# Kernel tuning notes

Hardware: AMD Instinct MI355X
Metric: run time of the kernel (lower is better)

The kernel has to match this reference:

```python
import jax, jax.numpy as jnp
import numpy as np

B = 512      # batch
H = 64       # latent_dim == GRU hidden size
F = 32       # n_features
S = 2048     # seq_len
NEG_SLOPE = 0.01  # nn.LeakyReLU default


def setup_inputs() -> dict:
    key = jax.random.key(0)
    ks = jax.random.split(key, 14)

    def p(k, shape, scale=0.1):
        return jax.random.normal(k, shape, dtype=jnp.float32) * scale

    return {
        "noise": jax.random.normal(ks[0], (B, H), dtype=jnp.float32),
        # GRU forward direction (layer 0): weight_ih_l0, weight_hh_l0, biases
        "W_ih_f": p(ks[1], (3 * H, H)),
        "W_hh_f": p(ks[2], (3 * H, H)),
        "b_ih_f": p(ks[3], (3 * H,)),
        "b_hh_f": p(ks[4], (3 * H,)),
        # GRU backward direction (layer 0 reverse)
        "W_ih_b": p(ks[5], (3 * H, H)),
        "W_hh_b": p(ks[6], (3 * H, H)),
        "b_ih_b": p(ks[7], (3 * H,)),
        "b_hh_b": p(ks[8], (3 * H,)),
        # latent_linear: Linear(2H -> H)
        "W_lat": p(ks[9], (H, 2 * H)),
        "b_lat": p(ks[10], (H,)),
        # output_linear: Linear(H -> F)
        "W_out": p(ks[11], (F, H)),
        "b_out": p(ks[12], (F,)),
    }


def _leaky(x):
    return jnp.where(x >= 0, x, NEG_SLOPE * x)


def _gru_cell(x, h, W_ih, W_hh, b_ih, b_hh):
    # PyTorch GRU cell: gates ordered (r, z, n)
    gi = x @ W_ih.T + b_ih          # (B, 3H)
    gh = h @ W_hh.T + b_hh          # (B, 3H)
    i_r, i_z, i_n = jnp.split(gi, 3, axis=-1)
    h_r, h_z, h_n = jnp.split(gh, 3, axis=-1)
    r = jax.nn.sigmoid(i_r + h_r)
    z = jax.nn.sigmoid(i_z + h_z)
    n = jnp.tanh(i_n + r * h_n)
    return (1.0 - z) * n + z * h


def reference(noise, W_ih_f, W_hh_f, b_ih_f, b_hh_f,
              W_ih_b, W_hh_b, b_ih_b, b_hh_b,
              W_lat, b_lat, W_out, b_out):
    # hidden_state = noise.repeat((D*n_layers,1,1)) -> both directions start at noise
    batch = noise.shape[0]

    def step(carry, _):
        x, hf, hb = carry
        # GRU on a length-1 sequence: each direction does one cell update;
        # output timestep = concat(fwd_out, bwd_out)
        hf2 = _gru_cell(x, hf, W_ih_f, W_hh_f, b_ih_f, b_hh_f)
        hb2 = _gru_cell(x, hb, W_ih_b, W_hh_b, b_ih_b, b_hh_b)
        out = jnp.concatenate([hf2, hb2], axis=-1)        # (B, 2H)
        lat = _leaky(out @ W_lat.T + b_lat)               # (B, H)
        return (lat, hf2, hb2), lat

    x0 = jnp.zeros((batch, H), dtype=noise.dtype)
    _, ys = jax.lax.scan(step, (x0, noise, noise), None, length=S)
    seq = jnp.transpose(ys, (1, 0, 2))   # (B, S, H)
    seq = _leaky(seq)                    # second LeakyReLU as in the original
    out = jax.nn.sigmoid(seq @ W_out.T + b_out)  # (B, S, F)
    return out
```

## Files before the change

### kernel.cpp

```cpp
#include <hip/hip_runtime.h>
#include <hip/hip_bf16.h>


#define NBATCH 512
#define NH 64
#define NS 2048
#define NF 32
#define MROW 16
#define LDH 72

typedef short s16x8 __attribute__((ext_vector_type(8)));
typedef float f32x4 __attribute__((ext_vector_type(4)));

#define MFMA(a, b, c) __builtin_amdgcn_mfma_f32_16x16x32_bf16((a), (b), (c), 0, 0, 0)

#define NLOG2E  (-1.4426950408889634f)
#define N2LOG2E (-2.8853900817779268f)

__device__ __forceinline__ void bar_nodrain() {
    asm volatile("s_barrier" ::: "memory");
}

__device__ __forceinline__ void bar_lgkm() {
    asm volatile("s_waitcnt lgkmcnt(0)\n\ts_barrier" ::: "memory");
}

__device__ __forceinline__ short f2bf(float f) {
    return (short)((__float_as_uint(f) + 0x8000u) >> 16);
}

__device__ __forceinline__ f32x4 v_exp2(f32x4 a) {
    f32x4 r;
#pragma unroll
    for (int i = 0; i < 4; ++i) r[i] = __builtin_amdgcn_exp2f(a[i]);
    return r;
}

__device__ __forceinline__ f32x4 v_rcp(f32x4 a) {
    f32x4 r;
#pragma unroll
    for (int i = 0; i < 4; ++i) r[i] = __builtin_amdgcn_rcpf(a[i]);
    return r;
}

__device__ __forceinline__ f32x4 v_lk(f32x4 a) {
    f32x4 b = a * 0.01f;
    f32x4 r;
#pragma unroll
    for (int i = 0; i < 4; ++i) r[i] = fmaxf(a[i], b[i]);
    return r;
}

__device__ __forceinline__ f32x4 v_sigm(f32x4 a) {
    return v_rcp(v_exp2(a * NLOG2E) + 1.0f);
}

__device__ __forceinline__ int2 pk4bf(f32x4 v) {
    union { __hip_bfloat162 b; int i; } lo, hi;
    float2 a; a.x = v[0]; a.y = v[1];
    float2 b; b.x = v[2]; b.y = v[3];
    lo.b = __float22bfloat162_rn(a);
    hi.b = __float22bfloat162_rn(b);
    int2 r; r.x = lo.i; r.y = hi.i;
    return r;
}

__device__ __forceinline__ s16x8 bfragW(const float* __restrict__ W, int ldk,
                                        int row, int kf, int quad) {
    const float* p = W + (size_t)row * ldk + kf * 32 + quad * 8;
    s16x8 r;
#pragma unroll
    for (int i = 0; i < 8; ++i) r[i] = f2bf(p[i]);
    return r;
}

__device__ __forceinline__ f32x4 bias4(const float* __restrict__ p) {
    const float4 v = *(const float4*)p;
    f32x4 r = {v.x, v.y, v.z, v.w};
    return r;
}

__global__ __launch_bounds__(768)
void grugan_kernel(const float* __restrict__ noise,
                   const float* __restrict__ Wihf, const float* __restrict__ Whhf,
                   const float* __restrict__ bihf, const float* __restrict__ bhhf,
                   const float* __restrict__ Wihb, const float* __restrict__ Whhb,
                   const float* __restrict__ bihb, const float* __restrict__ bhhb,
                   const float* __restrict__ Wlat, const float* __restrict__ blat,
                   const float* __restrict__ Wout, const float* __restrict__ bout,
                   float* __restrict__ out)
{
    __shared__ __align__(16) short Xs[2][MROW][LDH];
    __shared__ __align__(16) short X2s[2][MROW][LDH];
    __shared__ __align__(16) short Hs[2][2][MROW][LDH];

    const int tid  = threadIdx.x;
    const int wave = tid >> 6;
    const int lane = tid & 63;
    const int n    = lane & 15;
    const int quad = lane >> 4;
    const int row0 = blockIdx.x * MROW;

    for (int idx = tid; idx < MROW * LDH; idx += 768) (&Xs[0][0][0])[idx] = 0;
    f32x4 hreg = {0.f, 0.f, 0.f, 0.f};
    const int gdir = wave >> 2;
    const int gjq  = (wave & 3) * 16 + quad * 4;
    if (wave < 8) {
        const float4 nz = *(const float4*)&noise[(size_t)(row0 + n) * NH + gjq];
        hreg[0] = nz.x; hreg[1] = nz.y; hreg[2] = nz.z; hreg[3] = nz.w;
        *(int2*)&Hs[0][gdir][n][gjq] = pk4bf(hreg);
    }
    __syncthreads();

    if (wave < 8) {
        const int dir  = gdir;
        const int cb   = wave & 3;
        const int jrow = cb * 16 + n;
        const int jq   = gjq;
        const float* Wih = dir ? Wihb : Wihf;
        const float* Whh = dir ? Whhb : Whhf;
        const float* bih = dir ? bihb : bihf;
        const float* bhh = dir ? bhhb : bhhf;

        s16x8 wir0 = bfragW(Wih, NH,   0 + jrow, 0, quad);
        s16x8 wir1 = bfragW(Wih, NH,   0 + jrow, 1, quad);
        s16x8 wiz0 = bfragW(Wih, NH,  64 + jrow, 0, quad);
        s16x8 wiz1 = bfragW(Wih, NH,  64 + jrow, 1, quad);
        s16x8 win0 = bfragW(Wih, NH, 128 + jrow, 0, quad);
        s16x8 win1 = bfragW(Wih, NH, 128 + jrow, 1, quad);
        s16x8 whr0 = bfragW(Whh, NH,   0 + jrow, 0, quad);
        s16x8 whr1 = bfragW(Whh, NH,   0 + jrow, 1, quad);
        s16x8 whz0 = bfragW(Whh, NH,  64 + jrow, 0, quad);
        s16x8 whz1 = bfragW(Whh, NH,  64 + jrow, 1, quad);
        s16x8 whn0 = bfragW(Whh, NH, 128 + jrow, 0, quad);
        s16x8 whn1 = bfragW(Whh, NH, 128 + jrow, 1, quad);
        f32x4 initR, initZ;
        {
            f32x4 a = bias4(&bih[jq]),      b = bias4(&bhh[jq]);
            initR = a + b;
            f32x4 c = bias4(&bih[64 + jq]), d = bias4(&bhh[64 + jq]);
            initZ = c + d;
        }
        const f32x4 initN1 = bias4(&bih[128 + jq]);
        const f32x4 initN2 = bias4(&bhh[128 + jq]);

        f32x4 accR, accZ, accN2;
        {
            s16x8 ha0 = *(const s16x8*)&Hs[0][dir][n][quad * 8];
            s16x8 ha1 = *(const s16x8*)&Hs[0][dir][n][32 + quad * 8];
            accR  = MFMA(whr0, ha0, initR);  accR  = MFMA(whr1, ha1, accR);
            accZ  = MFMA(whz0, ha0, initZ);  accZ  = MFMA(whz1, ha1, accZ);
            accN2 = MFMA(whn0, ha0, initN2); accN2 = MFMA(whn1, ha1, accN2);
        }

#define GSTEP(HB) do {                                                          \
        s16x8 xa0 = *(const s16x8*)&Xs[HB][n][quad * 8];                        \
        s16x8 xa1 = *(const s16x8*)&Xs[HB][n][32 + quad * 8];                   \
        accR = MFMA(wir0, xa0, accR);   accR = MFMA(wir1, xa1, accR);           \
        accZ = MFMA(wiz0, xa0, accZ);   accZ = MFMA(wiz1, xa1, accZ);           \
        f32x4 accN1 = MFMA(win0, xa0, initN1);                                  \
        accN1 = MFMA(win1, xa1, accN1);                                         \
        f32x4 eR = v_exp2(accR * NLOG2E);                                       \
        f32x4 rr = v_rcp(eR + 1.0f);                                            \
        f32x4 u  = accN1 + rr * accN2;                                          \
        f32x4 eU = v_exp2(u * N2LOG2E);                                         \
        f32x4 eZ = v_exp2(accZ * NLOG2E);                                       \
        f32x4 numer = (eZ + hreg) + eU * (hreg - eZ);                           \
        f32x4 denom = (eU + 1.0f) * (eZ + 1.0f);                                \
        hreg = numer * v_rcp(denom);                                            \
        *(int2*)&Hs[(HB) ^ 1][dir][n][jq] = pk4bf(hreg);                        \
        __syncthreads();                                \
        {                                                                       \
            s16x8 ha0 = *(const s16x8*)&Hs[(HB) ^ 1][dir][n][quad * 8];         \
            s16x8 ha1 = *(const s16x8*)&Hs[(HB) ^ 1][dir][n][32 + quad * 8];    \
            accR  = MFMA(whr0, ha0, initR);  accR  = MFMA(whr1, ha1, accR);     \
            accZ  = MFMA(whz0, ha0, initZ);  accZ  = MFMA(whz1, ha1, accZ);     \
            accN2 = MFMA(whn0, ha0, initN2); accN2 = MFMA(whn1, ha1, accN2);    \
        }                                                                       \
        __syncthreads();                                \
    } while (0)

        for (int t = 0; t < NS; t += 2) {
            GSTEP(0);
            GSTEP(1);
        }
#undef GSTEP
    } else {
        const int lt = wave & 3;
        const int nq = lt * 16 + quad * 4;
        s16x8 wl0 = bfragW(Wlat, 2 * NH, lt * 16 + n, 0, quad);
        s16x8 wl1 = bfragW(Wlat, 2 * NH, lt * 16 + n, 1, quad);
        s16x8 wl2 = bfragW(Wlat, 2 * NH, lt * 16 + n, 2, quad);
        s16x8 wl3 = bfragW(Wlat, 2 * NH, lt * 16 + n, 3, quad);
        const f32x4 initL = bias4(&blat[lt * 16 + quad * 4]);

        s16x8 wo0 = {};
        s16x8 wo1 = {};
        f32x4 initO = {0.f, 0.f, 0.f, 0.f};
        float* orow = nullptr;
        if (lt < 2) {
            const int f0 = lt * 16;
            wo0   = bfragW(Wout, NH, f0 + n, 0, quad);
            wo1   = bfragW(Wout, NH, f0 + n, 1, quad);
            initO = bias4(&bout[f0 + quad * 4]);
            orow  = out + (size_t)(row0 + n) * (NS * NF) + f0 + quad * 4;
        }
        const f32x4 zero4 = {0.f, 0.f, 0.f, 0.f};

#define LOSTEP(HB, T) do {                                                      \
        if (lt < 2 && (T) > 0) {                                                \
                \
                 \
            s16x8 p0 = *(const s16x8*)&X2s[HB][n][quad * 8];                    \
            s16x8 p1 = *(const s16x8*)&X2s[HB][n][32 + quad * 8];               \
            f32x4 po = MFMA(wo0, p0, initO);                                    \
            po = MFMA(wo1, p1, po);                                             \
            *(f32x4*)(orow + (size_t)((T) - 1) * NF) = v_sigm(po);              \
        }                                                                       \
        bar_nodrain();        \
        s16x8 fa0 = *(const s16x8*)&Hs[(HB) ^ 1][0][n][quad * 8];               \
        s16x8 fa1 = *(const s16x8*)&Hs[(HB) ^ 1][0][n][32 + quad * 8];          \
        s16x8 ba0 = *(const s16x8*)&Hs[(HB) ^ 1][1][n][quad * 8];               \
        s16x8 ba1 = *(const s16x8*)&Hs[(HB) ^ 1][1][n][32 + quad * 8];          \
        f32x4 lac1 = MFMA(wl0, fa0, initL);                                     \
        lac1 = MFMA(wl1, fa1, lac1);                                            \
        f32x4 lac2 = MFMA(wl2, ba0, zero4);                                     \
        lac2 = MFMA(wl3, ba1, lac2);                                            \
        f32x4 la = v_lk(lac1 + lac2);                                           \
        *(int2*)&Xs[(HB) ^ 1][n][nq]  = pk4bf(la);                              \
        *(int2*)&X2s[(HB) ^ 1][n][nq] = pk4bf(v_lk(la));                        \
        bar_lgkm();                   \
    } while (0)

        for (int t = 0; t < NS; t += 2) {
            LOSTEP(0, t);
            LOSTEP(1, t + 1);
        }
#undef LOSTEP

        if (lt < 2) {
            s16x8 p0 = *(const s16x8*)&X2s[0][n][quad * 8];
            s16x8 p1 = *(const s16x8*)&X2s[0][n][32 + quad * 8];
            f32x4 po = MFMA(wo0, p0, initO);
            po = MFMA(wo1, p1, po);
            *(f32x4*)(orow + (size_t)(NS - 1) * NF) = v_sigm(po);
        }
    }
}

extern "C" void kernel_launch(void* const* d_in, const int* in_sizes, int n_in,
                              void* d_out, int out_size, void* d_ws, size_t ws_size,
                              hipStream_t stream) {
    const float* noise = (const float*)d_in[0];
    const float* Wihf  = (const float*)d_in[1];
    const float* Whhf  = (const float*)d_in[2];
    const float* bihf  = (const float*)d_in[3];
    const float* bhhf  = (const float*)d_in[4];
    const float* Wihb  = (const float*)d_in[5];
    const float* Whhb  = (const float*)d_in[6];
    const float* bihb  = (const float*)d_in[7];
    const float* bhhb  = (const float*)d_in[8];
    const float* Wlat  = (const float*)d_in[9];
    const float* blat  = (const float*)d_in[10];
    const float* Wout  = (const float*)d_in[11];
    const float* bout  = (const float*)d_in[12];

    grugan_kernel<<<dim3(NBATCH / MROW), dim3(768), 0, stream>>>(
        noise, Wihf, Whhf, bihf, bhhf, Wihb, Whhb, bihb, bhhb,
        Wlat, blat, Wout, bout, (float*)d_out);
}
```

Before: 1.627 ms.

## Store shared activations in MFMA fragment-major layout and drop duplicate X2 buffer

Rearranges the shared-memory tiles for hidden states and latent inputs into a fragment-major layout [frag][quad][row][8], so each lane's 16-byte MFMA operand read is contiguous and free of bank conflicts without padding. It also removes the second X2s buffer holding the doubly-LeakyReLU'd latent. The output waves now reapply LeakyReLU on the fly after reading Xs, which cuts one LDS store per step on the latent waves. The cost is extra unpack, compare and repack ALU work in the output path.

```diff
diff --git a/kernel.cpp b/kernel.cpp
--- a/kernel.cpp
+++ b/kernel.cpp
@@ -7,7 +7,6 @@
 #define NS 2048
 #define NF 32
 #define MROW 16
-#define LDH 72
 
 typedef short s16x8 __attribute__((ext_vector_type(8)));
 typedef float f32x4 __attribute__((ext_vector_type(4)));
@@ -63,6 +62,19 @@
     hi.b = __float22bfloat162_rn(b);
     int2 r; r.x = lo.i; r.y = hi.i;
     return r;
+}
+
+__device__ __forceinline__ s16x8 lk_frag(s16x8 v) {
+    f32x4 lo, hi;
+#pragma unroll
+    for (int i = 0; i < 4; ++i) {
+        lo[i] = __uint_as_float(((unsigned)(unsigned short)v[i]) << 16);
+        hi[i] = __uint_as_float(((unsigned)(unsigned short)v[i + 4]) << 16);
+    }
+    union { struct { int2 a, b; } p; s16x8 s; } u;
+    u.p.a = pk4bf(v_lk(lo));
+    u.p.b = pk4bf(v_lk(hi));
+    return u.s;
 }
 
 __device__ __forceinline__ s16x8 bfragW(const float* __restrict__ W, int ldk,
@@ -90,9 +102,8 @@
                    const float* __restrict__ Wout, const float* __restrict__ bout,
                    float* __restrict__ out)
 {
-    __shared__ __align__(16) short Xs[2][MROW][LDH];
-    __shared__ __align__(16) short X2s[2][MROW][LDH];
-    __shared__ __align__(16) short Hs[2][2][MROW][LDH];
+    __shared__ __align__(16) short Xs[2][2][4][16][8];
+    __shared__ __align__(16) short Hs[2][2][2][4][16][8];
 
     const int tid  = threadIdx.x;
     const int wave = tid >> 6;
@@ -101,21 +112,26 @@
     const int quad = lane >> 4;
     const int row0 = blockIdx.x * MROW;
 
-    for (int idx = tid; idx < MROW * LDH; idx += 768) (&Xs[0][0][0])[idx] = 0;
+    for (int idx = tid; idx < 2 * 4 * 16 * 8; idx += 768)
+        (&Xs[0][0][0][0][0])[idx] = 0;
+
     f32x4 hreg = {0.f, 0.f, 0.f, 0.f};
     const int gdir = wave >> 2;
-    const int gjq  = (wave & 3) * 16 + quad * 4;
+    const int gcb  = wave & 3;
+    const int gjq  = gcb * 16 + quad * 4;
+    const int wfrag = gcb >> 1;
+    const int wq    = ((gcb & 1) << 1) | (quad >> 1);
+    const int we    = (quad & 1) << 2;
     if (wave < 8) {
         const float4 nz = *(const float4*)&noise[(size_t)(row0 + n) * NH + gjq];
         hreg[0] = nz.x; hreg[1] = nz.y; hreg[2] = nz.z; hreg[3] = nz.w;
-        *(int2*)&Hs[0][gdir][n][gjq] = pk4bf(hreg);
+        *(int2*)&Hs[0][gdir][wfrag][wq][n][we] = pk4bf(hreg);
     }
     __syncthreads();
 
     if (wave < 8) {
         const int dir  = gdir;
-        const int cb   = wave & 3;
-        const int jrow = cb * 16 + n;
+        const int jrow = gcb * 16 + n;
         const int jq   = gjq;
         const float* Wih = dir ? Wihb : Wihf;
         const float* Whh = dir ? Whhb : Whhf;
@@ -146,16 +162,16 @@
 
         f32x4 accR, accZ, accN2;
         {
-            s16x8 ha0 = *(const s16x8*)&Hs[0][dir][n][quad * 8];
-            s16x8 ha1 = *(const s16x8*)&Hs[0][dir][n][32 + quad * 8];
+            s16x8 ha0 = *(const s16x8*)&Hs[0][dir][0][quad][n][0];
+            s16x8 ha1 = *(const s16x8*)&Hs[0][dir][1][quad][n][0];
             accR  = MFMA(whr0, ha0, initR);  accR  = MFMA(whr1, ha1, accR);
             accZ  = MFMA(whz0, ha0, initZ);  accZ  = MFMA(whz1, ha1, accZ);
             accN2 = MFMA(whn0, ha0, initN2); accN2 = MFMA(whn1, ha1, accN2);
         }
 
 #define GSTEP(HB) do {                                                          \
-        s16x8 xa0 = *(const s16x8*)&Xs[HB][n][quad * 8];                        \
-        s16x8 xa1 = *(const s16x8*)&Xs[HB][n][32 + quad * 8];                   \
+        s16x8 xa0 = *(const s16x8*)&Xs[HB][0][quad][n][0];                      \
+        s16x8 xa1 = *(const s16x8*)&Xs[HB][1][quad][n][0];                      \
         accR = MFMA(wir0, xa0, accR);   accR = MFMA(wir1, xa1, accR);           \
         accZ = MFMA(wiz0, xa0, accZ);   accZ = MFMA(wiz1, xa1, accZ);           \
         f32x4 accN1 = MFMA(win0, xa0, initN1);                                  \
@@ -168,11 +184,11 @@
         f32x4 numer = (eZ + hreg) + eU * (hreg - eZ);                           \
         f32x4 denom = (eU + 1.0f) * (eZ + 1.0f);                                \
         hreg = numer * v_rcp(denom);                                            \
-        *(int2*)&Hs[(HB) ^ 1][dir][n][jq] = pk4bf(hreg);                        \
+        *(int2*)&Hs[(HB) ^ 1][dir][wfrag][wq][n][we] = pk4bf(hreg);             \
         __syncthreads();                                \
         {                                                                       \
-            s16x8 ha0 = *(const s16x8*)&Hs[(HB) ^ 1][dir][n][quad * 8];         \
-            s16x8 ha1 = *(const s16x8*)&Hs[(HB) ^ 1][dir][n][32 + quad * 8];    \
+            s16x8 ha0 = *(const s16x8*)&Hs[(HB) ^ 1][dir][0][quad][n][0];       \
+            s16x8 ha1 = *(const s16x8*)&Hs[(HB) ^ 1][dir][1][quad][n][0];       \
             accR  = MFMA(whr0, ha0, initR);  accR  = MFMA(whr1, ha1, accR);     \
             accZ  = MFMA(whz0, ha0, initZ);  accZ  = MFMA(whz1, ha1, accZ);     \
             accN2 = MFMA(whn0, ha0, initN2); accN2 = MFMA(whn1, ha1, accN2);    \
@@ -187,12 +203,14 @@
 #undef GSTEP
     } else {
         const int lt = wave & 3;
-        const int nq = lt * 16 + quad * 4;
         s16x8 wl0 = bfragW(Wlat, 2 * NH, lt * 16 + n, 0, quad);
         s16x8 wl1 = bfragW(Wlat, 2 * NH, lt * 16 + n, 1, quad);
         s16x8 wl2 = bfragW(Wlat, 2 * NH, lt * 16 + n, 2, quad);
         s16x8 wl3 = bfragW(Wlat, 2 * NH, lt * 16 + n, 3, quad);
         const f32x4 initL = bias4(&blat[lt * 16 + quad * 4]);
+        const int lfrag = lt >> 1;
+        const int lq    = ((lt & 1) << 1) | (quad >> 1);
+        const int le    = (quad & 1) << 2;
 
         s16x8 wo0 = {};
         s16x8 wo1 = {};
@@ -209,26 +227,25 @@
 
 #define LOSTEP(HB, T) do {                                                      \
         if (lt < 2 && (T) > 0) {                                                \
-                \
                  \
-            s16x8 p0 = *(const s16x8*)&X2s[HB][n][quad * 8];                    \
-            s16x8 p1 = *(const s16x8*)&X2s[HB][n][32 + quad * 8];               \
+                  \
+            s16x8 p0 = lk_frag(*(const s16x8*)&Xs[HB][0][quad][n][0]);          \
+            s16x8 p1 = lk_frag(*(const s16x8*)&Xs[HB][1][quad][n][0]);          \
             f32x4 po = MFMA(wo0, p0, initO);                                    \
             po = MFMA(wo1, p1, po);                                             \
             *(f32x4*)(orow + (size_t)((T) - 1) * NF) = v_sigm(po);              \
         }                                                                       \
         bar_nodrain();        \
-        s16x8 fa0 = *(const s16x8*)&Hs[(HB) ^ 1][0][n][quad * 8];               \
-        s16x8 fa1 = *(const s16x8*)&Hs[(HB) ^ 1][0][n][32 + quad * 8];          \
-        s16x8 ba0 = *(const s16x8*)&Hs[(HB) ^ 1][1][n][quad * 8];               \
-        s16x8 ba1 = *(const s16x8*)&Hs[(HB) ^ 1][1][n][32 + quad * 8];          \
+        s16x8 fa0 = *(const s16x8*)&Hs[(HB) ^ 1][0][0][quad][n][0];             \
+        s16x8 fa1 = *(const s16x8*)&Hs[(HB) ^ 1][0][1][quad][n][0];             \
+        s16x8 ba0 = *(const s16x8*)&Hs[(HB) ^ 1][1][0][quad][n][0];             \
+        s16x8 ba1 = *(const s16x8*)&Hs[(HB) ^ 1][1][1][quad][n][0];             \
         f32x4 lac1 = MFMA(wl0, fa0, initL);                                     \
         lac1 = MFMA(wl1, fa1, lac1);                                            \
         f32x4 lac2 = MFMA(wl2, ba0, zero4);                                     \
         lac2 = MFMA(wl3, ba1, lac2);                                            \
         f32x4 la = v_lk(lac1 + lac2);                                           \
-        *(int2*)&Xs[(HB) ^ 1][n][nq]  = pk4bf(la);                              \
-        *(int2*)&X2s[(HB) ^ 1][n][nq] = pk4bf(v_lk(la));                        \
+        *(int2*)&Xs[(HB) ^ 1][lfrag][lq][n][le] = pk4bf(la);                    \
         bar_lgkm();                   \
     } while (0)
 
@@ -239,8 +256,8 @@
 #undef LOSTEP
 
         if (lt < 2) {
-            s16x8 p0 = *(const s16x8*)&X2s[0][n][quad * 8];
-            s16x8 p1 = *(const s16x8*)&X2s[0][n][32 + quad * 8];
+            s16x8 p0 = lk_frag(*(const s16x8*)&Xs[0][0][quad][n][0]);
+            s16x8 p1 = lk_frag(*(const s16x8*)&Xs[0][1][quad][n][0]);
             f32x4 po = MFMA(wo0, p0, initO);
             po = MFMA(wo1, p1, po);
             *(f32x4*)(orow + (size_t)(NS - 1) * NF) = v_sigm(po);
```

New measurement: 1.721 ms. +5.8%, slower.

## Merge latent-linear into GRU waves, redundantly computed per wave to cut barriers

Applied to the files above, without the earlier changes.

Removes the four dedicated latent/output waves and has every GRU wave compute the full latent projection redundantly in registers. The fragment-permuted Wlat rows make the MFMA output land directly in the next step's input-fragment layout. The shared H buffer is relaid out so fragments load without padding. This cuts each timestep from two barriers plus a producer-consumer hop to a single barrier. In exchange each wave issues 16 extra MFMAs per step and holds many more weight registers, and output stores now sit on the critical path of waves 0-1.

```diff
diff --git a/kernel.cpp b/kernel.cpp
--- a/kernel.cpp
+++ b/kernel.cpp
@@ -7,7 +7,6 @@
 #define NS 2048
 #define NF 32
 #define MROW 16
-#define LDH 72
 
 typedef short s16x8 __attribute__((ext_vector_type(8)));
 typedef float f32x4 __attribute__((ext_vector_type(4)));
@@ -16,10 +15,6 @@
 
 #define NLOG2E  (-1.4426950408889634f)
 #define N2LOG2E (-2.8853900817779268f)
-
-__device__ __forceinline__ void bar_nodrain() {
-    asm volatile("s_barrier" ::: "memory");
-}
 
 __device__ __forceinline__ void bar_lgkm() {
     asm volatile("s_waitcnt lgkmcnt(0)\n\ts_barrier" ::: "memory");
@@ -65,6 +60,12 @@
     return r;
 }
 
+__device__ __forceinline__ s16x8 pack2(int2 a, int2 b) {
+    union { struct { int2 a, b; } p; s16x8 s; } u;
+    u.p.a = a; u.p.b = b;
+    return u.s;
+}
+
 __device__ __forceinline__ s16x8 bfragW(const float* __restrict__ W, int ldk,
                                         int row, int kf, int quad) {
     const float* p = W + (size_t)row * ldk + kf * 32 + quad * 8;
@@ -80,7 +81,7 @@
     return r;
 }
 
-__global__ __launch_bounds__(768)
+__global__ __launch_bounds__(512)
 void grugan_kernel(const float* __restrict__ noise,
                    const float* __restrict__ Wihf, const float* __restrict__ Whhf,
                    const float* __restrict__ bihf, const float* __restrict__ bhhf,
@@ -90,9 +91,7 @@
                    const float* __restrict__ Wout, const float* __restrict__ bout,
                    float* __restrict__ out)
 {
-    __shared__ __align__(16) short Xs[2][MROW][LDH];
-    __shared__ __align__(16) short X2s[2][MROW][LDH];
-    __shared__ __align__(16) short Hs[2][2][MROW][LDH];
+    __shared__ __align__(16) short Hs[2][2][2][4][16][8];
 
     const int tid  = threadIdx.x;
     const int wave = tid >> 6;
@@ -101,61 +100,98 @@
     const int quad = lane >> 4;
     const int row0 = blockIdx.x * MROW;
 
-    for (int idx = tid; idx < MROW * LDH; idx += 768) (&Xs[0][0][0])[idx] = 0;
-    f32x4 hreg = {0.f, 0.f, 0.f, 0.f};
-    const int gdir = wave >> 2;
-    const int gjq  = (wave & 3) * 16 + quad * 4;
-    if (wave < 8) {
-        const float4 nz = *(const float4*)&noise[(size_t)(row0 + n) * NH + gjq];
+    const int dir = wave >> 2;
+    const int cb  = wave & 3;
+    const int jq  = cb * 16 + quad * 4;
+    const int wfrag = cb >> 1;
+    const int wq    = ((cb & 1) << 1) | (quad >> 1);
+    const int we    = (quad & 1) << 2;
+
+    const int jrow = cb * 16 + n;
+    const float* Wih = dir ? Wihb : Wihf;
+    const float* Whh = dir ? Whhb : Whhf;
+    const float* bih = dir ? bihb : bihf;
+    const float* bhh = dir ? bhhb : bhhf;
+
+    s16x8 wir0 = bfragW(Wih, NH,   0 + jrow, 0, quad);
+    s16x8 wir1 = bfragW(Wih, NH,   0 + jrow, 1, quad);
+    s16x8 wiz0 = bfragW(Wih, NH,  64 + jrow, 0, quad);
+    s16x8 wiz1 = bfragW(Wih, NH,  64 + jrow, 1, quad);
+    s16x8 win0 = bfragW(Wih, NH, 128 + jrow, 0, quad);
+    s16x8 win1 = bfragW(Wih, NH, 128 + jrow, 1, quad);
+    s16x8 whr0 = bfragW(Whh, NH,   0 + jrow, 0, quad);
+    s16x8 whr1 = bfragW(Whh, NH,   0 + jrow, 1, quad);
+    s16x8 whz0 = bfragW(Whh, NH,  64 + jrow, 0, quad);
+    s16x8 whz1 = bfragW(Whh, NH,  64 + jrow, 1, quad);
+    s16x8 whn0 = bfragW(Whh, NH, 128 + jrow, 0, quad);
+    s16x8 whn1 = bfragW(Whh, NH, 128 + jrow, 1, quad);
+
+    f32x4 initR, initZ;
+    {
+        f32x4 a = bias4(&bih[jq]),      b = bias4(&bhh[jq]);
+        initR = a + b;
+        f32x4 c = bias4(&bih[64 + jq]), d = bias4(&bhh[64 + jq]);
+        initZ = c + d;
+    }
+    const f32x4 initN1 = bias4(&bih[128 + jq]);
+    const f32x4 initN2 = bias4(&bhh[128 + jq]);
+
+    const int prow = 8 * (n >> 2) + (n & 3);
+    s16x8 wlA0 = bfragW(Wlat, 2 * NH, prow,      0, quad);
+    s16x8 wlA1 = bfragW(Wlat, 2 * NH, prow,      1, quad);
+    s16x8 wlA2 = bfragW(Wlat, 2 * NH, prow,      2, quad);
+    s16x8 wlA3 = bfragW(Wlat, 2 * NH, prow,      3, quad);
+    s16x8 wlB0 = bfragW(Wlat, 2 * NH, prow + 4,  0, quad);
+    s16x8 wlB1 = bfragW(Wlat, 2 * NH, prow + 4,  1, quad);
+    s16x8 wlB2 = bfragW(Wlat, 2 * NH, prow + 4,  2, quad);
+    s16x8 wlB3 = bfragW(Wlat, 2 * NH, prow + 4,  3, quad);
+    s16x8 wlC0 = bfragW(Wlat, 2 * NH, prow + 32, 0, quad);
+    s16x8 wlC1 = bfragW(Wlat, 2 * NH, prow + 32, 1, quad);
+    s16x8 wlC2 = bfragW(Wlat, 2 * NH, prow + 32, 2, quad);
+    s16x8 wlC3 = bfragW(Wlat, 2 * NH, prow + 32, 3, quad);
+    s16x8 wlD0 = bfragW(Wlat, 2 * NH, prow + 36, 0, quad);
+    s16x8 wlD1 = bfragW(Wlat, 2 * NH, prow + 36, 1, quad);
+    s16x8 wlD2 = bfragW(Wlat, 2 * NH, prow + 36, 2, quad);
+    s16x8 wlD3 = bfragW(Wlat, 2 * NH, prow + 36, 3, quad);
+    const f32x4 initXA = bias4(&blat[ 0 + 8 * quad]);
+    const f32x4 initXB = bias4(&blat[ 4 + 8 * quad]);
+    const f32x4 initXC = bias4(&blat[32 + 8 * quad]);
+    const f32x4 initXD = bias4(&blat[36 + 8 * quad]);
+
+    s16x8 wo0 = {};
+    s16x8 wo1 = {};
+    f32x4 initO = {0.f, 0.f, 0.f, 0.f};
+    float* orow = nullptr;
+    if (wave < 2) {
+        const int f0 = wave * 16;
+        wo0   = bfragW(Wout, NH, f0 + n, 0, quad);
+        wo1   = bfragW(Wout, NH, f0 + n, 1, quad);
+        initO = bias4(&bout[f0 + quad * 4]);
+        orow  = out + (size_t)(row0 + n) * (NS * NF) + f0 + quad * 4;
+    }
+    const f32x4 zero4 = {0.f, 0.f, 0.f, 0.f};
+
+    f32x4 hreg;
+    {
+        const float4 nz = *(const float4*)&noise[(size_t)(row0 + n) * NH + jq];
         hreg[0] = nz.x; hreg[1] = nz.y; hreg[2] = nz.z; hreg[3] = nz.w;
-        *(int2*)&Hs[0][gdir][n][gjq] = pk4bf(hreg);
+        *(int2*)&Hs[0][dir][wfrag][wq][n][we] = pk4bf(hreg);
     }
     __syncthreads();
 
-    if (wave < 8) {
-        const int dir  = gdir;
-        const int cb   = wave & 3;
-        const int jrow = cb * 16 + n;
-        const int jq   = gjq;
-        const float* Wih = dir ? Wihb : Wihf;
-        const float* Whh = dir ? Whhb : Whhf;
-        const float* bih = dir ? bihb : bihf;
-        const float* bhh = dir ? bhhb : bhhf;
-
-        s16x8 wir0 = bfragW(Wih, NH,   0 + jrow, 0, quad);
-        s16x8 wir1 = bfragW(Wih, NH,   0 + jrow, 1, quad);
-        s16x8 wiz0 = bfragW(Wih, NH,  64 + jrow, 0, quad);
-        s16x8 wiz1 = bfragW(Wih, NH,  64 + jrow, 1, quad);
-        s16x8 win0 = bfragW(Wih, NH, 128 + jrow, 0, quad);
-        s16x8 win1 = bfragW(Wih, NH, 128 + jrow, 1, quad);
-        s16x8 whr0 = bfragW(Whh, NH,   0 + jrow, 0, quad);
-        s16x8 whr1 = bfragW(Whh, NH,   0 + jrow, 1, quad);
-        s16x8 whz0 = bfragW(Whh, NH,  64 + jrow, 0, quad);
-        s16x8 whz1 = bfragW(Whh, NH,  64 + jrow, 1, quad);
-        s16x8 whn0 = bfragW(Whh, NH, 128 + jrow, 0, quad);
-        s16x8 whn1 = bfragW(Whh, NH, 128 + jrow, 1, quad);
-        f32x4 initR, initZ;
-        {
-            f32x4 a = bias4(&bih[jq]),      b = bias4(&bhh[jq]);
-            initR = a + b;
-            f32x4 c = bias4(&bih[64 + jq]), d = bias4(&bhh[64 + jq]);
-            initZ = c + d;
-        }
-        const f32x4 initN1 = bias4(&bih[128 + jq]);
-        const f32x4 initN2 = bias4(&bhh[128 + jq]);
-
-        f32x4 accR, accZ, accN2;
-        {
-            s16x8 ha0 = *(const s16x8*)&Hs[0][dir][n][quad * 8];
-            s16x8 ha1 = *(const s16x8*)&Hs[0][dir][n][32 + quad * 8];
-            accR  = MFMA(whr0, ha0, initR);  accR  = MFMA(whr1, ha1, accR);
-            accZ  = MFMA(whz0, ha0, initZ);  accZ  = MFMA(whz1, ha1, accZ);
-            accN2 = MFMA(whn0, ha0, initN2); accN2 = MFMA(whn1, ha1, accN2);
-        }
-
-#define GSTEP(HB) do {                                                          \
-        s16x8 xa0 = *(const s16x8*)&Xs[HB][n][quad * 8];                        \
-        s16x8 xa1 = *(const s16x8*)&Xs[HB][n][32 + quad * 8];                   \
+    f32x4 accR, accZ, accN2;
+    {
+        s16x8 h00 = *(const s16x8*)&Hs[0][dir][0][quad][n][0];
+        s16x8 h01 = *(const s16x8*)&Hs[0][dir][1][quad][n][0];
+        accR  = MFMA(whr0, h00, initR);  accR  = MFMA(whr1, h01, accR);
+        accZ  = MFMA(whz0, h00, initZ);  accZ  = MFMA(whz1, h01, accZ);
+        accN2 = MFMA(whn0, h00, initN2); accN2 = MFMA(whn1, h01, accN2);
+    }
+    s16x8 xa0 = {};
+    s16x8 xa1 = {};
+
+#define STEP(PB, T) do {                                                        \
+              \
         accR = MFMA(wir0, xa0, accR);   accR = MFMA(wir1, xa1, accR);           \
         accZ = MFMA(wiz0, xa0, accZ);   accZ = MFMA(wiz1, xa1, accZ);           \
         f32x4 accN1 = MFMA(win0, xa0, initN1);                                  \
@@ -168,84 +204,54 @@
         f32x4 numer = (eZ + hreg) + eU * (hreg - eZ);                           \
         f32x4 denom = (eU + 1.0f) * (eZ + 1.0f);                                \
         hreg = numer * v_rcp(denom);                                            \
-        *(int2*)&Hs[(HB) ^ 1][dir][n][jq] = pk4bf(hreg);                        \
-        __syncthreads();                                \
+        *(int2*)&Hs[PB][dir][wfrag][wq][n][we] = pk4bf(hreg);                   \
+        bar_lgkm();                            \
+                 \
+        s16x8 hf0 = *(const s16x8*)&Hs[PB][0][0][quad][n][0];                   \
+        s16x8 hf1 = *(const s16x8*)&Hs[PB][0][1][quad][n][0];                   \
+        s16x8 hb0 = *(const s16x8*)&Hs[PB][1][0][quad][n][0];                   \
+        s16x8 hb1 = *(const s16x8*)&Hs[PB][1][1][quad][n][0];                   \
+        f32x4 la, lb, lc, ld;                                                   \
         {                                                                       \
-            s16x8 ha0 = *(const s16x8*)&Hs[(HB) ^ 1][dir][n][quad * 8];         \
-            s16x8 ha1 = *(const s16x8*)&Hs[(HB) ^ 1][dir][n][32 + quad * 8];    \
+            f32x4 pA = MFMA(wlA0, hf0, initXA); pA = MFMA(wlA1, hf1, pA);       \
+            f32x4 qA = MFMA(wlA2, hb0, zero4);  qA = MFMA(wlA3, hb1, qA);       \
+            la = pA + qA;                                                       \
+            f32x4 pB = MFMA(wlB0, hf0, initXB); pB = MFMA(wlB1, hf1, pB);       \
+            f32x4 qB = MFMA(wlB2, hb0, zero4);  qB = MFMA(wlB3, hb1, qB);       \
+            lb = pB + qB;                                                       \
+            f32x4 pC = MFMA(wlC0, hf0, initXC); pC = MFMA(wlC1, hf1, pC);       \
+            f32x4 qC = MFMA(wlC2, hb0, zero4);  qC = MFMA(wlC3, hb1, qC);       \
+            lc = pC + qC;                                                       \
+            f32x4 pD = MFMA(wlD0, hf0, initXD); pD = MFMA(wlD1, hf1, pD);       \
+            f32x4 qD = MFMA(wlD2, hb0, zero4);  qD = MFMA(wlD3, hb1, qD);       \
+            ld = pD + qD;                                                       \
+        }                                                                       \
+        f32x4 xA = v_lk(la), xB = v_lk(lb), xC = v_lk(lc), xD = v_lk(ld);       \
+        xa0 = pack2(pk4bf(xA), pk4bf(xB));                                      \
+        xa1 = pack2(pk4bf(xC), pk4bf(xD));                                      \
+        {                                                                       \
+            s16x8 ha0 = dir ? hb0 : hf0;                                        \
+            s16x8 ha1 = dir ? hb1 : hf1;                                        \
             accR  = MFMA(whr0, ha0, initR);  accR  = MFMA(whr1, ha1, accR);     \
             accZ  = MFMA(whz0, ha0, initZ);  accZ  = MFMA(whz1, ha1, accZ);     \
             accN2 = MFMA(whn0, ha0, initN2); accN2 = MFMA(whn1, ha1, accN2);    \
         }                                                                       \
-        __syncthreads();                                \
+        if (wave < 2) {                                                         \
+              \
+                          \
+            s16x8 xo0 = pack2(pk4bf(v_lk(xA)), pk4bf(v_lk(xB)));                \
+            s16x8 xo1 = pack2(pk4bf(v_lk(xC)), pk4bf(v_lk(xD)));                \
+            f32x4 po = MFMA(wo0, xo0, initO);                                   \
+            po = MFMA(wo1, xo1, po);                                            \
+            *(f32x4*)(orow + (size_t)(T) * NF) = v_sigm(po);                    \
+        }                                                                       \
     } while (0)
 
-        for (int t = 0; t < NS; t += 2) {
-            GSTEP(0);
-            GSTEP(1);
-        }
-#undef GSTEP
-    } else {
-        const int lt = wave & 3;
-        const int nq = lt * 16 + quad * 4;
-        s16x8 wl0 = bfragW(Wlat, 2 * NH, lt * 16 + n, 0, quad);
-        s16x8 wl1 = bfragW(Wlat, 2 * NH, lt * 16 + n, 1, quad);
-        s16x8 wl2 = bfragW(Wlat, 2 * NH, lt * 16 + n, 2, quad);
-        s16x8 wl3 = bfragW(Wlat, 2 * NH, lt * 16 + n, 3, quad);
-        const f32x4 initL = bias4(&blat[lt * 16 + quad * 4]);
-
-        s16x8 wo0 = {};
-        s16x8 wo1 = {};
-        f32x4 initO = {0.f, 0.f, 0.f, 0.f};
-        float* orow = nullptr;
-        if (lt < 2) {
-            const int f0 = lt * 16;
-            wo0   = bfragW(Wout, NH, f0 + n, 0, quad);
-            wo1   = bfragW(Wout, NH, f0 + n, 1, quad);
-            initO = bias4(&bout[f0 + quad * 4]);
-            orow  = out + (size_t)(row0 + n) * (NS * NF) + f0 + quad * 4;
-        }
-        const f32x4 zero4 = {0.f, 0.f, 0.f, 0.f};
-
-#define LOSTEP(HB, T) do {                                                      \
-        if (lt < 2 && (T) > 0) {                                                \
-                \
-                 \
-            s16x8 p0 = *(const s16x8*)&X2s[HB][n][quad * 8];                    \
-            s16x8 p1 = *(const s16x8*)&X2s[HB][n][32 + quad * 8];               \
-            f32x4 po = MFMA(wo0, p0, initO);                                    \
-            po = MFMA(wo1, p1, po);                                             \
-            *(f32x4*)(orow + (size_t)((T) - 1) * NF) = v_sigm(po);              \
-        }                                                                       \
-        bar_nodrain();        \
-        s16x8 fa0 = *(const s16x8*)&Hs[(HB) ^ 1][0][n][quad * 8];               \
-        s16x8 fa1 = *(const s16x8*)&Hs[(HB) ^ 1][0][n][32 + quad * 8];          \
-        s16x8 ba0 = *(const s16x8*)&Hs[(HB) ^ 1][1][n][quad * 8];               \
-        s16x8 ba1 = *(const s16x8*)&Hs[(HB) ^ 1][1][n][32 + quad * 8];          \
-        f32x4 lac1 = MFMA(wl0, fa0, initL);                                     \
-        lac1 = MFMA(wl1, fa1, lac1);                                            \
-        f32x4 lac2 = MFMA(wl2, ba0, zero4);                                     \
-        lac2 = MFMA(wl3, ba1, lac2);                                            \
-        f32x4 la = v_lk(lac1 + lac2);                                           \
-        *(int2*)&Xs[(HB) ^ 1][n][nq]  = pk4bf(la);                              \
-        *(int2*)&X2s[(HB) ^ 1][n][nq] = pk4bf(v_lk(la));                        \
-        bar_lgkm();                   \
-    } while (0)
-
-        for (int t = 0; t < NS; t += 2) {
-            LOSTEP(0, t);
-            LOSTEP(1, t + 1);
-        }
-#undef LOSTEP
-
-        if (lt < 2) {
-            s16x8 p0 = *(const s16x8*)&X2s[0][n][quad * 8];
-            s16x8 p1 = *(const s16x8*)&X2s[0][n][32 + quad * 8];
-            f32x4 po = MFMA(wo0, p0, initO);
-            po = MFMA(wo1, p1, po);
-            *(f32x4*)(orow + (size_t)(NS - 1) * NF) = v_sigm(po);
-        }
-    }
+    for (int t = 0; t < NS; t += 2) {
+        STEP(1, t);
+        STEP(0, t + 1);
+    }
+#undef STEP
 }
 
 extern "C" void kernel_launch(void* const* d_in, const int* in_sizes, int n_in,
@@ -265,7 +271,7 @@
     const float* Wout  = (const float*)d_in[11];
     const float* bout  = (const float*)d_in[12];
 
-    grugan_kernel<<<dim3(NBATCH / MROW), dim3(768), 0, stream>>>(
+    grugan_kernel<<<dim3(NBATCH / MROW), dim3(512), 0, stream>>>(
         noise, Wihf, Whhf, bihf, bhhf, Wihb, Whhb, bihb, bhhb,
         Wlat, blat, Wout, bout, (float*)d_out);
 }
```

Measured after the change: 2.524 ms. +55.1%, slower.
